# Kernel tuning notes

Measured on AMD Instinct MI355X. Metric: run time of the kernel, lower is better.

## Reference

```python
import jax, jax.numpy as jnp
import numpy as np

HIDDEN = 1024
HEADS = 16
HEAD_DIM = HIDDEN // HEADS
B, S = 2, 2048


def setup_inputs() -> dict:
    key = jax.random.key(0)
    k1, k2, k3 = jax.random.split(key, 3)
    scale_in = 1.0 / np.sqrt(HIDDEN)
    x = jax.random.normal(k1, (B, S, HIDDEN), dtype=jnp.float32)
    wqkv_w = jax.random.normal(k2, (3 * HIDDEN, HIDDEN), dtype=jnp.float32) * scale_in
    wo_w = jax.random.normal(k3, (HIDDEN, HIDDEN), dtype=jnp.float32) * scale_in
    wo_b = jnp.zeros((HIDDEN,), dtype=jnp.float32)
    return {"x": x, "wqkv_w": wqkv_w, "wo_w": wo_w, "wo_b": wo_b}


def reference(x, wqkv_w, wo_w, wo_b):
    b, s, d = x.shape
    h, hd = HEADS, HEAD_DIM
    sm_scale = hd ** (-0.5)
    # QKV projection (torch Linear: x @ W^T), then chunk into q,k,v
    qkv = jnp.einsum('bsd,ed->bse', x, wqkv_w)  # [b, s, 3d]
    q, k, v = jnp.split(qkv, 3, axis=-1)
    # [b, h, s, hd]
    q = q.reshape(b, s, h, hd).transpose(0, 2, 1, 3)
    k = k.reshape(b, s, h, hd).transpose(0, 2, 1, 3)
    v = v.reshape(b, s, h, hd).transpose(0, 2, 1, 3)
    # raw scores, then causal mask (mask applied BEFORE scaling, as in source;
    # -inf * scale == -inf so math matches softmax(score*scale) with mask)
    scores = jnp.einsum('bhqe,bhke->bhqk', q, k)
    causal = jnp.tril(jnp.ones((s, s), dtype=bool))
    scores = jnp.where(causal[None, None, :, :], scores, -jnp.inf)
    weights = jax.nn.softmax(scores * sm_scale, axis=-1)
    # dropout p=0.0 (eval) -> identity
    out = jnp.einsum('bhqk,bhke->bhqe', weights, v)
    out = out.transpose(0, 2, 1, 3).reshape(b, s, h * hd)
    y = jnp.einsum('bsd,ed->bse', out, wo_w) + wo_b
    return (y, k, v)
```

## Files before the change

kernel.cpp:

```cpp
#include <hip/hip_runtime.h>
#include <cstdint>
#include <cstddef>


using bf16x8 = __attribute__((ext_vector_type(8))) __bf16;
using f32x4  = __attribute__((ext_vector_type(4))) float;
using u16    = unsigned short;

#define SOFT_SCALE 0.1803368801111244f

__device__ __forceinline__ u16 f2bf(float f) {
  union { float f; uint32_t u; } a; a.f = f;
  uint32_t r = a.u + 0x7fffu + ((a.u >> 16) & 1u);
  return (u16)(r >> 16);
}

__device__ __forceinline__ bf16x8 ldfrag(const u16* p) {
  return *reinterpret_cast<const bf16x8*>(p);
}

__device__ __forceinline__ void gload_lds16(const void* g, void* l) {
  __builtin_amdgcn_global_load_lds((const __attribute__((address_space(1))) void*)g,
                                   (__attribute__((address_space(3))) void*)l,
                                   16, 0, 0);
}

__device__ __forceinline__ uint32_t cvt_pk_bf16(float a, float b) {
  uint32_t r;
  asm("v_cvt_pk_bf16_f32 %0, %1, %2" : "=v"(r) : "v"(a), "v"(b));
  return r;
}

__global__ void cvt_all(const float* __restrict__ x, const float* __restrict__ wqkv,
                        const float* __restrict__ wo,
                        u16* __restrict__ xb, u16* __restrict__ wqkvb, u16* __restrict__ wob) {
  int i = blockIdx.x * blockDim.x + threadIdx.x;
  int stride = gridDim.x * blockDim.x;
  for (; i < 2097152; i += stride) {
    const float* src; u16* dst; int j;
    if (i < 1048576)      { src = x;    dst = xb;    j = i; }
    else if (i < 1835008) { src = wqkv; dst = wqkvb; j = i - 1048576; }
    else                  { src = wo;   dst = wob;   j = i - 1835008; }
    float4 v = reinterpret_cast<const float4*>(src)[j];
    ushort4 o;
    o.x = f2bf(v.x); o.y = f2bf(v.y); o.z = f2bf(v.z); o.w = f2bf(v.w);
    reinterpret_cast<ushort4*>(dst)[j] = o;
  }
}

__global__ __launch_bounds__(512, 2) void qkv_gemm_kernel(
    const u16* __restrict__ Xb, const u16* __restrict__ Wb,
    u16* __restrict__ Qws, u16* __restrict__ Kws, u16* __restrict__ Vtws,
    float* __restrict__ out) {
  extern __shared__ char smem[];

  const int tid = threadIdx.x, lane = tid & 63, wid = tid >> 6;
  const int wr = wid >> 2, wc = wid & 3;
  const int fq = lane >> 4, fr = lane & 15;

  const int wg = (blockIdx.x & 7) * 24 + (blockIdx.x >> 3);
  const int bm = wg / 12, bn = wg % 12;
  const int m0 = bm * 256, n0 = bn * 256;

  const char* Ab = (const char*)Xb + (size_t)m0 * 2048;
  const char* Bb = (const char*)Wb + (size_t)n0 * 2048;

  f32x4 acc[8][4] = {};

  auto stage_half = [&](int t, int mat, int h) {
    char* dst = smem + mat * 65536 + (t & 1) * 32768 + h * 16384;
    const char* src = mat ? Bb : Ab;
#pragma unroll
    for (int l = 0; l < 2; ++l) {
      int lin = (l * 512 + tid) * 16;
      int rl  = lin >> 7;
      int col = (lin & 127) ^ ((rl & 7) << 4);
      gload_lds16(src + (size_t)(h * 128 + rl) * 2048 + t * 128 + col, dst + lin);
    }
  };

  stage_half(0, 0, 0); stage_half(0, 0, 1);
  stage_half(0, 1, 0); stage_half(0, 1, 1);
  stage_half(1, 1, 0); stage_half(1, 1, 1);
  asm volatile("s_waitcnt vmcnt(4)" ::: "memory");
  __builtin_amdgcn_s_barrier();

  bf16x8 afr[4][2];
  bf16x8 bfr[4][2];

  for (int t = 0; t < 16; ++t) {
    const char* As = smem + (t & 1) * 32768;
    const char* Bs = smem + 65536 + (t & 1) * 32768;

#pragma unroll
    for (int m = 0; m < 4; ++m) {
      int row = wr * 128 + m * 16 + fr;
#pragma unroll
      for (int ks = 0; ks < 2; ++ks)
        afr[m][ks] = *(const bf16x8*)(As + row * 128 + ((ks * 64 + fq * 16) ^ ((row & 7) << 4)));
    }
#pragma unroll
    for (int n = 0; n < 2; ++n) {
      int row = wc * 64 + n * 16 + fr;
#pragma unroll
      for (int ks = 0; ks < 2; ++ks)
        bfr[n][ks] = *(const bf16x8*)(Bs + row * 128 + ((ks * 64 + fq * 16) ^ ((row & 7) << 4)));
    }
    if (t + 1 < 16) stage_half(t + 1, 0, 0);
    __builtin_amdgcn_s_barrier();
    asm volatile("s_waitcnt lgkmcnt(0)" ::: "memory");
    __builtin_amdgcn_sched_barrier(0);
    __builtin_amdgcn_s_setprio(1);
#pragma unroll
    for (int m = 0; m < 4; ++m)
#pragma unroll
      for (int n = 0; n < 2; ++n)
#pragma unroll
        for (int ks = 0; ks < 2; ++ks)
          acc[m][n] = __builtin_amdgcn_mfma_f32_16x16x32_bf16(afr[m][ks], bfr[n][ks], acc[m][n], 0, 0, 0);
    __builtin_amdgcn_s_setprio(0);
    __builtin_amdgcn_s_barrier();

#pragma unroll
    for (int n = 2; n < 4; ++n) {
      int row = wc * 64 + n * 16 + fr;
#pragma unroll
      for (int ks = 0; ks < 2; ++ks)
        bfr[n][ks] = *(const bf16x8*)(Bs + row * 128 + ((ks * 64 + fq * 16) ^ ((row & 7) << 4)));
    }
    if (t + 1 < 16) stage_half(t + 1, 0, 1);
    __builtin_amdgcn_s_barrier();
    asm volatile("s_waitcnt lgkmcnt(0)" ::: "memory");
    __builtin_amdgcn_sched_barrier(0);
    __builtin_amdgcn_s_setprio(1);
#pragma unroll
    for (int m = 0; m < 4; ++m)
#pragma unroll
      for (int n = 2; n < 4; ++n)
#pragma unroll
        for (int ks = 0; ks < 2; ++ks)
          acc[m][n] = __builtin_amdgcn_mfma_f32_16x16x32_bf16(afr[m][ks], bfr[n][ks], acc[m][n], 0, 0, 0);
    __builtin_amdgcn_s_setprio(0);
    __builtin_amdgcn_s_barrier();

#pragma unroll
    for (int m = 0; m < 4; ++m) {
      int row = wr * 128 + (m + 4) * 16 + fr;
#pragma unroll
      for (int ks = 0; ks < 2; ++ks)
        afr[m][ks] = *(const bf16x8*)(As + row * 128 + ((ks * 64 + fq * 16) ^ ((row & 7) << 4)));
    }
    if (t + 2 < 16) stage_half(t + 2, 1, 0);
    __builtin_amdgcn_s_barrier();
    asm volatile("s_waitcnt lgkmcnt(0)" ::: "memory");
    __builtin_amdgcn_sched_barrier(0);
    __builtin_amdgcn_s_setprio(1);
#pragma unroll
    for (int m = 0; m < 4; ++m)
#pragma unroll
      for (int n = 0; n < 2; ++n)
#pragma unroll
        for (int ks = 0; ks < 2; ++ks)
          acc[m + 4][n] = __builtin_amdgcn_mfma_f32_16x16x32_bf16(afr[m][ks], bfr[n][ks], acc[m + 4][n], 0, 0, 0);
    __builtin_amdgcn_s_setprio(0);
    __builtin_amdgcn_s_barrier();

    if (t + 2 < 16) stage_half(t + 2, 1, 1);
    __builtin_amdgcn_s_barrier();
    __builtin_amdgcn_s_setprio(1);
#pragma unroll
    for (int m = 0; m < 4; ++m)
#pragma unroll
      for (int n = 2; n < 4; ++n)
#pragma unroll
        for (int ks = 0; ks < 2; ++ks)
          acc[m + 4][n] = __builtin_amdgcn_mfma_f32_16x16x32_bf16(afr[m][ks], bfr[n][ks], acc[m + 4][n], 0, 0, 0);
    __builtin_amdgcn_s_setprio(0);
    if (t < 15) {
      if (t == 14) asm volatile("s_waitcnt vmcnt(0)" ::: "memory");
      else         asm volatile("s_waitcnt vmcnt(4)" ::: "memory");
    }
    __builtin_amdgcn_s_barrier();
  }

  const int sect = n0 >> 10;
  const int nn0 = (n0 & 1023) + wc * 64;
  const int mbase = m0 + wr * 128;
#pragma unroll
  for (int m = 0; m < 8; ++m)
#pragma unroll
    for (int n = 0; n < 4; ++n) {
      int mB = mbase + m * 16 + fq * 4;
      int ncol = nn0 + n * 16 + fr;
      int b = mB >> 11, s0 = mB & 2047;
      int h = ncol >> 6, hd = ncol & 63;
      size_t base = (((size_t)b * 16 + h) * 2048 + s0) * 64 + hd;
      float v0 = acc[m][n][0], v1 = acc[m][n][1], v2 = acc[m][n][2], v3 = acc[m][n][3];
      if (sect == 0) {
        Qws[base]       = f2bf(v0 * SOFT_SCALE);
        Qws[base + 64]  = f2bf(v1 * SOFT_SCALE);
        Qws[base + 128] = f2bf(v2 * SOFT_SCALE);
        Qws[base + 192] = f2bf(v3 * SOFT_SCALE);
      } else if (sect == 1) {
        Kws[base] = f2bf(v0); Kws[base + 64] = f2bf(v1);
        Kws[base + 128] = f2bf(v2); Kws[base + 192] = f2bf(v3);
        out[4194304 + base] = v0; out[4194304 + base + 64] = v1;
        out[4194304 + base + 128] = v2; out[4194304 + base + 192] = v3;
      } else {
        out[8388608 + base] = v0; out[8388608 + base + 64] = v1;
        out[8388608 + base + 128] = v2; out[8388608 + base + 192] = v3;
        size_t tt = ((size_t)(b * 16 + h) * 64 + hd) * 2048 + s0;
        ushort4 pk; pk.x = f2bf(v0); pk.y = f2bf(v1); pk.z = f2bf(v2); pk.w = f2bf(v3);
        *reinterpret_cast<ushort4*>(Vtws + tt) = pk;
      }
    }
}

__device__ __forceinline__ void gemm128_core(const u16* __restrict__ A,
                                             const u16* __restrict__ B,
                                             int m0, int n0, int K,
                                             u16* As, u16* Bs, f32x4 acc[4][4]) {
  const int tid  = threadIdx.x;
  const int lane = tid & 63;
  const int wid  = tid >> 6;
  const int wr = wid >> 1, wc = wid & 1;
  const int fq = lane >> 4, fr = lane & 15;

  for (int kb = 0; kb < K; kb += 32) {
#pragma unroll
    for (int j = 0; j < 2; ++j) {
      int lin = (j * 256 + tid) * 16;
      int row = lin >> 6;
      int rb  = lin & 63;
      gload_lds16((const char*)(A + (size_t)(m0 + row) * K + kb) + rb, (char*)As + lin);
      gload_lds16((const char*)(B + (size_t)(n0 + row) * K + kb) + rb, (char*)Bs + lin);
    }
    __syncthreads();

    bf16x8 av[4], bv[4];
#pragma unroll
    for (int i = 0; i < 4; ++i) av[i] = ldfrag(As + (wr * 64 + i * 16 + fr) * 32 + fq * 8);
#pragma unroll
    for (int j = 0; j < 4; ++j) bv[j] = ldfrag(Bs + (wc * 64 + j * 16 + fr) * 32 + fq * 8);
    __builtin_amdgcn_s_setprio(1);
#pragma unroll
    for (int i = 0; i < 4; ++i)
#pragma unroll
      for (int j = 0; j < 4; ++j)
        acc[i][j] = __builtin_amdgcn_mfma_f32_16x16x32_bf16(av[i], bv[j], acc[i][j], 0, 0, 0);
    __builtin_amdgcn_s_setprio(0);
    __syncthreads();
  }
}

__global__ __launch_bounds__(256, 4) void attn_kernel(
    const u16* __restrict__ Qw, const u16* __restrict__ Kw,
    const u16* __restrict__ Vtw, u16* __restrict__ Ow) {
  __shared__ u16 Ks[2][64 * 64];
  __shared__ u16 Vs[2][64 * 64];

  const int tid = threadIdx.x, lane = tid & 63, wid = tid >> 6;
  const int fq = lane >> 4, fr = lane & 15;
  const int bh = blockIdx.x & 31;
  const int qb = 31 - (blockIdx.x >> 5);
  const int b = bh >> 4, h = bh & 15;
  const int q0 = qb * 64;

  const u16* Qbase  = Qw  + (size_t)bh * 2048 * 64;
  const u16* Kbase  = Kw  + (size_t)bh * 2048 * 64;
  const char* VtBase = (const char*)(Vtw + (size_t)bh * 64 * 2048);

#pragma unroll
  for (int f = 0; f < 2; ++f) {
    int lin = (f * 256 + tid) * 16;
    int row = lin >> 7;
    int logical = lin ^ ((row & 7) << 4);
    gload_lds16((const char*)Kbase + logical, (char*)Ks[0] + lin);
    gload_lds16(VtBase + (size_t)row * 4096 + (logical & 127), (char*)Vs[0] + lin);
  }

  const int qrow = q0 + wid * 16 + fr;
  bf16x8 qa0 = ldfrag(Qbase + (size_t)qrow * 64 + fq * 8);
  bf16x8 qa1 = ldfrag(Qbase + (size_t)qrow * 64 + 32 + fq * 8);

  float ssum = 0.f;
  f32x4 accO[4] = {};

  int cur = 0;
  for (int kb = 0; kb <= qb; ++kb) {
    __syncthreads();

    if (kb < qb) {
      const char* kg = (const char*)(Kbase + (size_t)(kb + 1) * 64 * 64);
#pragma unroll
      for (int f = 0; f < 2; ++f) {
        int lin = (f * 256 + tid) * 16;
        int row = lin >> 7;
        int logical = lin ^ ((row & 7) << 4);
        gload_lds16(kg + logical, (char*)Ks[cur ^ 1] + lin);
        gload_lds16(VtBase + (size_t)row * 4096 + (size_t)(kb + 1) * 128 + (logical & 127),
                    (char*)Vs[cur ^ 1] + lin);
      }
    }

    const u16* Kc = Ks[cur];
    const u16* Vc = Vs[cur];

    f32x4 sfr[4];
    __builtin_amdgcn_s_setprio(1);
#pragma unroll
    for (int n = 0; n < 4; ++n) {
      int krow = n * 16 + fr;
      bf16x8 kf0 = ldfrag(Kc + krow * 64 + ((fq * 8)      ^ ((krow & 7) << 3)));
      bf16x8 kf1 = ldfrag(Kc + krow * 64 + ((fq * 8 + 32) ^ ((krow & 7) << 3)));
      f32x4 z = {};
      z = __builtin_amdgcn_mfma_f32_16x16x32_bf16(kf0, qa0, z, 0, 0, 0);
      z = __builtin_amdgcn_mfma_f32_16x16x32_bf16(kf1, qa1, z, 0, 0, 0);
      sfr[n] = z;
    }
    __builtin_amdgcn_s_setprio(0);

    uint32_t W[4][2];
#pragma unroll
    for (int n = 0; n < 4; ++n) {
      float p0, p1, p2, p3;
      if (kb < qb) {
        p0 = exp2f(sfr[n][0]);
        p1 = exp2f(sfr[n][1]);
        p2 = exp2f(sfr[n][2]);
        p3 = exp2f(sfr[n][3]);
      } else {
        int kvg = kb * 64 + n * 16 + fq * 4;
        p0 = (kvg + 0 > qrow) ? 0.f : exp2f(sfr[n][0]);
        p1 = (kvg + 1 > qrow) ? 0.f : exp2f(sfr[n][1]);
        p2 = (kvg + 2 > qrow) ? 0.f : exp2f(sfr[n][2]);
        p3 = (kvg + 3 > qrow) ? 0.f : exp2f(sfr[n][3]);
      }
      ssum += (p0 + p1) + (p2 + p3);
      W[n][0] = cvt_pk_bf16(p0, p1);
      W[n][1] = cvt_pk_bf16(p2, p3);
    }

    union { uint32_t u[4]; bf16x8 v; } pa0u, pa1u;
#pragma unroll
    for (int hh = 0; hh < 2; ++hh) {
      uint32_t a0 = W[0][hh], b0 = W[1][hh];
      asm("v_permlane32_swap_b32 %0, %1" : "+v"(a0), "+v"(b0));
      asm("v_permlane16_swap_b32 %0, %1" : "+v"(a0), "+v"(b0));
      pa0u.u[hh] = a0; pa0u.u[2 + hh] = b0;
      uint32_t a1 = W[2][hh], b1 = W[3][hh];
      asm("v_permlane32_swap_b32 %0, %1" : "+v"(a1), "+v"(b1));
      asm("v_permlane16_swap_b32 %0, %1" : "+v"(a1), "+v"(b1));
      pa1u.u[hh] = a1; pa1u.u[2 + hh] = b1;
    }

    __builtin_amdgcn_s_setprio(1);
#pragma unroll
    for (int nh = 0; nh < 4; ++nh) {
      int vrow = nh * 16 + fr;
      bf16x8 vb0 = ldfrag(Vc + vrow * 64 + ((fq * 8)      ^ ((vrow & 7) << 3)));
      bf16x8 vb1 = ldfrag(Vc + vrow * 64 + ((fq * 8 + 32) ^ ((vrow & 7) << 3)));
      accO[nh] = __builtin_amdgcn_mfma_f32_16x16x32_bf16(pa0u.v, vb0, accO[nh], 0, 0, 0);
      accO[nh] = __builtin_amdgcn_mfma_f32_16x16x32_bf16(pa1u.v, vb1, accO[nh], 0, 0, 0);
    }
    __builtin_amdgcn_s_setprio(0);
    cur ^= 1;
  }

  ssum += __shfl_xor(ssum, 16);
  ssum += __shfl_xor(ssum, 32);
  float inv = 1.0f / ssum;
  float invq[4];
#pragma unroll
  for (int r = 0; r < 4; ++r) invq[r] = __shfl(inv, fq * 4 + r);

#pragma unroll
  for (int nh = 0; nh < 4; ++nh)
#pragma unroll
    for (int r = 0; r < 4; ++r) {
      float o = accO[nh][r] * invq[r];
      int qr = q0 + wid * 16 + fq * 4 + r;
      Ow[((size_t)b * 2048 + qr) * 1024 + h * 64 + nh * 16 + fr] = f2bf(o);
    }
}

__global__ __launch_bounds__(256) void proj_gemm_kernel(
    const u16* __restrict__ Ob, const u16* __restrict__ Wob,
    const float* __restrict__ bias, float* __restrict__ out) {
  __shared__ u16 As[128 * 32];
  __shared__ u16 Bs[128 * 32];
  const int NB = 8;
  int m0 = (blockIdx.x / NB) * 128, n0 = (blockIdx.x % NB) * 128;
  f32x4 acc[4][4] = {};
  gemm128_core(Ob, Wob, m0, n0, 1024, As, Bs, acc);

  const int lane = threadIdx.x & 63, wid = threadIdx.x >> 6;
  const int wr = wid >> 1, wc = wid & 1, fq = lane >> 4, fr = lane & 15;
#pragma unroll
  for (int i = 0; i < 4; ++i)
#pragma unroll
    for (int j = 0; j < 4; ++j)
#pragma unroll
      for (int r = 0; r < 4; ++r) {
        int m = m0 + wr * 64 + i * 16 + fq * 4 + r;
        int n = n0 + wc * 64 + j * 16 + fr;
        out[(size_t)m * 1024 + n] = acc[i][j][r] + bias[n];
      }
}

extern "C" void kernel_launch(void* const* d_in, const int* in_sizes, int n_in,
                              void* d_out, int out_size, void* d_ws, size_t ws_size,
                              hipStream_t stream) {
  const float* x    = (const float*)d_in[0];
  const float* wqkv = (const float*)d_in[1];
  const float* wo   = (const float*)d_in[2];
  const float* wo_b = (const float*)d_in[3];
  float* out = (float*)d_out;

  u16* xb    = (u16*)d_ws;
  u16* wqkvb = xb    + 4194304;
  u16* wob   = wqkvb + 3145728;
  u16* q_ws  = wob   + 1048576;
  u16* k_ws  = q_ws  + 4194304;
  u16* vt_ws = k_ws  + 4194304;
  u16* o_ws  = vt_ws + 4194304;

  static bool attr_set = false;
  if (!attr_set) {
    hipFuncSetAttribute((const void*)qkv_gemm_kernel,
                        hipFuncAttributeMaxDynamicSharedMemorySize, 131072);
    attr_set = true;
  }

  cvt_all<<<2048, 256, 0, stream>>>(x, wqkv, wo, xb, wqkvb, wob);
  qkv_gemm_kernel<<<192, 512, 131072, stream>>>(xb, wqkvb, q_ws, k_ws, vt_ws, out);
  attn_kernel<<<32 * 32, 256, 0, stream>>>(q_ws, k_ws, vt_ws, o_ws);
  proj_gemm_kernel<<<32 * 8, 256, 0, stream>>>(o_ws, wob, wo_b, out);
}
```

Baseline: 117.8 us.

## Split attention waves into 2x2 query/KV tiles with LDS reduction

Each of the four waves now owns 32 query rows and half of the 64-key block (a 2x2 split) instead of 16 query rows against all 64 keys. Each K and V fragment loaded from LDS now feeds two MFMAs, which roughly halves LDS fragment traffic per block. The two KV-half partial outputs and row sums are combined at the end through LDS, reusing the K/V buffers, before normalisation and the store. This adds an extra barrier pair, an LDS reduction, and more live accumulator registers per wave.

```diff
diff --git a/kernel.cpp b/kernel.cpp
--- a/kernel.cpp
+++ b/kernel.cpp
@@ -260,6 +260,7 @@
   __shared__ u16 Vs[2][64 * 64];
 
   const int tid = threadIdx.x, lane = tid & 63, wid = tid >> 6;
+  const int wk = wid >> 1, wh = wid & 1;
   const int fq = lane >> 4, fr = lane & 15;
   const int bh = blockIdx.x & 31;
   const int qb = 31 - (blockIdx.x >> 5);
@@ -279,12 +280,15 @@
     gload_lds16(VtBase + (size_t)row * 4096 + (logical & 127), (char*)Vs[0] + lin);
   }
 
-  const int qrow = q0 + wid * 16 + fr;
-  bf16x8 qa0 = ldfrag(Qbase + (size_t)qrow * 64 + fq * 8);
-  bf16x8 qa1 = ldfrag(Qbase + (size_t)qrow * 64 + 32 + fq * 8);
-
-  float ssum = 0.f;
-  f32x4 accO[4] = {};
+  bf16x8 qa[2][2];
+#pragma unroll
+  for (int qt = 0; qt < 2; ++qt)
+#pragma unroll
+    for (int kh = 0; kh < 2; ++kh)
+      qa[qt][kh] = ldfrag(Qbase + (size_t)(q0 + wh * 32 + qt * 16 + fr) * 64 + kh * 32 + fq * 8);
+
+  float ssum[2] = {0.f, 0.f};
+  f32x4 accO[2][4] = {};
 
   int cur = 0;
   for (int kb = 0; kb <= qb; ++kb) {
@@ -306,82 +310,121 @@
     const u16* Kc = Ks[cur];
     const u16* Vc = Vs[cur];
 
-    f32x4 sfr[4];
-    __builtin_amdgcn_s_setprio(1);
-#pragma unroll
-    for (int n = 0; n < 4; ++n) {
-      int krow = n * 16 + fr;
+    f32x4 st[2][2];
+    __builtin_amdgcn_s_setprio(1);
+#pragma unroll
+    for (int kvt = 0; kvt < 2; ++kvt) {
+      int krow = wk * 32 + kvt * 16 + fr;
       bf16x8 kf0 = ldfrag(Kc + krow * 64 + ((fq * 8)      ^ ((krow & 7) << 3)));
       bf16x8 kf1 = ldfrag(Kc + krow * 64 + ((fq * 8 + 32) ^ ((krow & 7) << 3)));
-      f32x4 z = {};
-      z = __builtin_amdgcn_mfma_f32_16x16x32_bf16(kf0, qa0, z, 0, 0, 0);
-      z = __builtin_amdgcn_mfma_f32_16x16x32_bf16(kf1, qa1, z, 0, 0, 0);
-      sfr[n] = z;
-    }
-    __builtin_amdgcn_s_setprio(0);
-
-    uint32_t W[4][2];
-#pragma unroll
-    for (int n = 0; n < 4; ++n) {
-      float p0, p1, p2, p3;
-      if (kb < qb) {
-        p0 = exp2f(sfr[n][0]);
-        p1 = exp2f(sfr[n][1]);
-        p2 = exp2f(sfr[n][2]);
-        p3 = exp2f(sfr[n][3]);
-      } else {
-        int kvg = kb * 64 + n * 16 + fq * 4;
-        p0 = (kvg + 0 > qrow) ? 0.f : exp2f(sfr[n][0]);
-        p1 = (kvg + 1 > qrow) ? 0.f : exp2f(sfr[n][1]);
-        p2 = (kvg + 2 > qrow) ? 0.f : exp2f(sfr[n][2]);
-        p3 = (kvg + 3 > qrow) ? 0.f : exp2f(sfr[n][3]);
-      }
-      ssum += (p0 + p1) + (p2 + p3);
-      W[n][0] = cvt_pk_bf16(p0, p1);
-      W[n][1] = cvt_pk_bf16(p2, p3);
-    }
-
-    union { uint32_t u[4]; bf16x8 v; } pa0u, pa1u;
-#pragma unroll
-    for (int hh = 0; hh < 2; ++hh) {
-      uint32_t a0 = W[0][hh], b0 = W[1][hh];
-      asm("v_permlane32_swap_b32 %0, %1" : "+v"(a0), "+v"(b0));
-      asm("v_permlane16_swap_b32 %0, %1" : "+v"(a0), "+v"(b0));
-      pa0u.u[hh] = a0; pa0u.u[2 + hh] = b0;
-      uint32_t a1 = W[2][hh], b1 = W[3][hh];
-      asm("v_permlane32_swap_b32 %0, %1" : "+v"(a1), "+v"(b1));
-      asm("v_permlane16_swap_b32 %0, %1" : "+v"(a1), "+v"(b1));
-      pa1u.u[hh] = a1; pa1u.u[2 + hh] = b1;
-    }
-
-    __builtin_amdgcn_s_setprio(1);
-#pragma unroll
-    for (int nh = 0; nh < 4; ++nh) {
-      int vrow = nh * 16 + fr;
-      bf16x8 vb0 = ldfrag(Vc + vrow * 64 + ((fq * 8)      ^ ((vrow & 7) << 3)));
-      bf16x8 vb1 = ldfrag(Vc + vrow * 64 + ((fq * 8 + 32) ^ ((vrow & 7) << 3)));
-      accO[nh] = __builtin_amdgcn_mfma_f32_16x16x32_bf16(pa0u.v, vb0, accO[nh], 0, 0, 0);
-      accO[nh] = __builtin_amdgcn_mfma_f32_16x16x32_bf16(pa1u.v, vb1, accO[nh], 0, 0, 0);
+#pragma unroll
+      for (int qt = 0; qt < 2; ++qt) {
+        f32x4 z = {};
+        z = __builtin_amdgcn_mfma_f32_16x16x32_bf16(kf0, qa[qt][0], z, 0, 0, 0);
+        z = __builtin_amdgcn_mfma_f32_16x16x32_bf16(kf1, qa[qt][1], z, 0, 0, 0);
+        st[kvt][qt] = z;
+      }
+    }
+    __builtin_amdgcn_s_setprio(0);
+
+    uint32_t W[2][2][2];
+#pragma unroll
+    for (int qt = 0; qt < 2; ++qt) {
+      int qrow = q0 + wh * 32 + qt * 16 + fr;
+#pragma unroll
+      for (int kvt = 0; kvt < 2; ++kvt) {
+        float p0, p1, p2, p3;
+        if (kb < qb) {
+          p0 = exp2f(st[kvt][qt][0]);
+          p1 = exp2f(st[kvt][qt][1]);
+          p2 = exp2f(st[kvt][qt][2]);
+          p3 = exp2f(st[kvt][qt][3]);
+        } else {
+          int kvg = kb * 64 + wk * 32 + kvt * 16 + fq * 4;
+          p0 = (kvg + 0 > qrow) ? 0.f : exp2f(st[kvt][qt][0]);
+          p1 = (kvg + 1 > qrow) ? 0.f : exp2f(st[kvt][qt][1]);
+          p2 = (kvg + 2 > qrow) ? 0.f : exp2f(st[kvt][qt][2]);
+          p3 = (kvg + 3 > qrow) ? 0.f : exp2f(st[kvt][qt][3]);
+        }
+        ssum[qt] += (p0 + p1) + (p2 + p3);
+        W[qt][kvt][0] = cvt_pk_bf16(p0, p1);
+        W[qt][kvt][1] = cvt_pk_bf16(p2, p3);
+      }
+    }
+
+    union U { uint32_t u[4]; bf16x8 v; };
+    U pa[2];
+#pragma unroll
+    for (int qt = 0; qt < 2; ++qt)
+#pragma unroll
+      for (int hh = 0; hh < 2; ++hh) {
+        uint32_t a0 = W[qt][0][hh], b0 = W[qt][1][hh];
+        asm("v_permlane32_swap_b32 %0, %1" : "+v"(a0), "+v"(b0));
+        asm("v_permlane16_swap_b32 %0, %1" : "+v"(a0), "+v"(b0));
+        pa[qt].u[hh] = a0; pa[qt].u[2 + hh] = b0;
+      }
+
+    __builtin_amdgcn_s_setprio(1);
+#pragma unroll
+    for (int ht = 0; ht < 4; ++ht) {
+      int vrow = ht * 16 + fr;
+      bf16x8 vb = ldfrag(Vc + vrow * 64 + ((wk * 32 + fq * 8) ^ ((vrow & 7) << 3)));
+#pragma unroll
+      for (int qt = 0; qt < 2; ++qt)
+        accO[qt][ht] = __builtin_amdgcn_mfma_f32_16x16x32_bf16(pa[qt].v, vb, accO[qt][ht], 0, 0, 0);
     }
     __builtin_amdgcn_s_setprio(0);
     cur ^= 1;
   }
 
-  ssum += __shfl_xor(ssum, 16);
-  ssum += __shfl_xor(ssum, 32);
-  float inv = 1.0f / ssum;
-  float invq[4];
-#pragma unroll
-  for (int r = 0; r < 4; ++r) invq[r] = __shfl(inv, fq * 4 + r);
-
-#pragma unroll
-  for (int nh = 0; nh < 4; ++nh)
-#pragma unroll
-    for (int r = 0; r < 4; ++r) {
-      float o = accO[nh][r] * invq[r];
-      int qr = q0 + wid * 16 + fq * 4 + r;
-      Ow[((size_t)b * 2048 + qr) * 1024 + h * 64 + nh * 16 + fr] = f2bf(o);
-    }
+#pragma unroll
+  for (int qt = 0; qt < 2; ++qt) {
+    ssum[qt] += __shfl_xor(ssum[qt], 16);
+    ssum[qt] += __shfl_xor(ssum[qt], 32);
+  }
+
+  __syncthreads();
+  float* Ored = (float*)Ks;
+  float* Sred = (float*)Vs;
+  if (wk == 1) {
+#pragma unroll
+    for (int qt = 0; qt < 2; ++qt)
+#pragma unroll
+      for (int ht = 0; ht < 4; ++ht)
+        *reinterpret_cast<f32x4*>(&Ored[(((wh * 2 + qt) * 4 + ht) << 8) + lane * 4]) = accO[qt][ht];
+    if (fq == 0) {
+      Sred[wh * 64 + fr]      = ssum[0];
+      Sred[wh * 64 + 16 + fr] = ssum[1];
+    }
+  }
+  __syncthreads();
+  if (wk == 0) {
+#pragma unroll
+    for (int qt = 0; qt < 2; ++qt)
+#pragma unroll
+      for (int ht = 0; ht < 4; ++ht) {
+        f32x4 o = *reinterpret_cast<const f32x4*>(&Ored[(((wh * 2 + qt) * 4 + ht) << 8) + lane * 4]);
+        accO[qt][ht] += o;
+      }
+    float invq[2][4];
+#pragma unroll
+    for (int qt = 0; qt < 2; ++qt) {
+      float s = ssum[qt] + Sred[wh * 64 + qt * 16 + fr];
+      float inv = 1.0f / s;
+#pragma unroll
+      for (int r = 0; r < 4; ++r) invq[qt][r] = __shfl(inv, fq * 4 + r);
+    }
+#pragma unroll
+    for (int qt = 0; qt < 2; ++qt)
+#pragma unroll
+      for (int ht = 0; ht < 4; ++ht)
+#pragma unroll
+        for (int r = 0; r < 4; ++r) {
+          float o = accO[qt][ht][r] * invq[qt][r];
+          int qr = q0 + wh * 32 + qt * 16 + fq * 4 + r;
+          Ow[((size_t)b * 2048 + qr) * 1024 + h * 64 + ht * 16 + fr] = f2bf(o);
+        }
+  }
 }
 
 __global__ __launch_bounds__(256) void proj_gemm_kernel(
```

Result: no change. 116.5 us (-1.1%).
